# Optimization experiments

Measured on AMD Instinct MI355X. Metric: run time of the kernel, lower is better.

## Reference

```python
import jax, jax.numpy as jnp
import numpy as np

N, E, D_FEAT, D_HID, N_CLASS, N_LAYER = 100000, 1600000, 128, 128, 40, 2


def _sage_layer(x, x_, src, dst, wl, wr, b, n):
    # mean aggregation of neighbor (src) features into dst nodes
    agg = jax.ops.segment_sum(x[src], dst, num_segments=n)          # [N, d_in]
    cnt = jax.ops.segment_sum(jnp.ones((src.shape[0], 1), x.dtype), dst, num_segments=n)
    agg = agg / jnp.maximum(cnt, 1.0)
    h = agg @ wl + x @ wr + b        # neighbor path + root path
    h_ = x_ @ wr + b                 # twin (detached-root) stream: root weight only
    return jax.nn.relu(h), jax.nn.relu(h_)


def setup_inputs() -> dict:
    key = jax.random.key(0)
    ks = jax.random.split(key, 12)
    s = 1.0 / np.sqrt(D_HID)
    inp = {
        "x": jax.random.normal(ks[0], (N, D_FEAT), jnp.float32),
        "edge_index1": jax.random.randint(ks[1], (2, E), 0, N, jnp.int32),
        "edge_index2": jax.random.randint(ks[2], (2, E), 0, N, jnp.int32),
        "wl1": jax.random.uniform(ks[3], (D_FEAT, D_HID), jnp.float32, -s, s),
        "wr1": jax.random.uniform(ks[4], (D_FEAT, D_HID), jnp.float32, -s, s),
        "b1": jnp.zeros((D_HID,), jnp.float32),
        "wl2": jax.random.uniform(ks[5], (D_HID, D_HID), jnp.float32, -s, s),
        "wr2": jax.random.uniform(ks[6], (D_HID, D_HID), jnp.float32, -s, s),
        "b2": jnp.zeros((D_HID,), jnp.float32),
        "w_out": jax.random.uniform(ks[7], (D_HID * N_LAYER, N_CLASS), jnp.float32, -s, s),
        "b_out": jnp.zeros((N_CLASS,), jnp.float32),
        "batch_size": N,
    }
    return inp


def reference(x, edge_index1, edge_index2, wl1, wr1, b1, wl2, wr2, b2, w_out, b_out, batch_size):
    n = x.shape[0]
    x_ = jax.lax.stop_gradient(x)[:batch_size]   # detached twin stream of root nodes
    # layer 1 (dropout is eval-mode no-op)
    h1, h1_ = _sage_layer(x, x_, edge_index1[0], edge_index1[1], wl1, wr1, b1, n)
    # layer 2
    h2, h2_ = _sage_layer(h1, h1_, edge_index2[0], edge_index2[1], wl2, wr2, b2, n)
    # jumping knowledge: mode 'cat' over per-layer root representations
    h = jnp.concatenate([h1[:batch_size], h2[:batch_size]], axis=-1)
    return h @ w_out + b_out
```

## Files before the change

### kernel.cpp

```cpp
#include <hip/hip_runtime.h>


#define MAXB  512
#define CAP   24
#define CAPS  6144
#define PBLK  384

typedef __attribute__((ext_vector_type(8))) short short8;
typedef __attribute__((ext_vector_type(4))) float floatx4;

__device__ __forceinline__ unsigned short f2b(float f) {
    unsigned u = __float_as_uint(f);
    unsigned r = (u + 0x7fffu + ((u >> 16) & 1u)) >> 16;
    return (unsigned short)r;
}
__device__ __forceinline__ float lo2f(unsigned u) { return __uint_as_float(u << 16); }
__device__ __forceinline__ float hi2f(unsigned u) { return __uint_as_float(u & 0xffff0000u); }
__device__ __forceinline__ unsigned pack2(float a, float b) {
    return (unsigned)f2b(a) | ((unsigned)f2b(b) << 16);
}

__global__ __launch_bounds__(256)
void prep_all(const float4* __restrict__ x4, uint4* __restrict__ xb4, long n8,
              const float* __restrict__ wl1, const float* __restrict__ wr1,
              const float* __restrict__ wl2, const float* __restrict__ wr2,
              const float* __restrict__ wo,
              unsigned short* __restrict__ wt1, unsigned short* __restrict__ wt2,
              unsigned short* __restrict__ wot, int* __restrict__ zero_region) {
    long i = (long)blockIdx.x * 256 + threadIdx.x;
    if (i < 2048) zero_region[i] = 0;
    if (i < n8) {
        float4 a = x4[i * 2];
        float4 b = x4[i * 2 + 1];
        uint4 o;
        o.x = pack2(a.x, a.y); o.y = pack2(a.z, a.w);
        o.z = pack2(b.x, b.y); o.w = pack2(b.z, b.w);
        xb4[i] = o;
    }
    if (i < 65536) {
        int l = (int)(i >> 15);
        int k5 = (int)(i & 32767);
        int j = k5 & 7, lane = (k5 >> 3) & 63, kb = (k5 >> 9) & 7, c = k5 >> 12;
        int k = kb * 32 + (lane >> 4) * 8 + j;
        int n = c * 16 + (lane & 15);
        const float* Wl = l ? wl2 : wl1;
        const float* Wr = l ? wr2 : wr1;
        float v = (k < 128) ? Wl[k * 128 + n] : Wr[(k - 128) * 128 + n];
        (l ? wt2 : wt1)[k5] = f2b(v);
    } else if (i < 65536 + 12288) {
        int k5 = (int)(i - 65536);
        int j = k5 & 7, lane = (k5 >> 3) & 63, kb = (k5 >> 9) & 7, c = k5 >> 12;
        int k = kb * 32 + (lane >> 4) * 8 + j;
        int col = c * 16 + (lane & 15);
        float v = (col < 40) ? wo[k * 40 + col] : 0.0f;
        wot[k5] = f2b(v);
    }
}

__global__ __launch_bounds__(256)
void bucket_hist2(const int* __restrict__ dst1, const int* __restrict__ dst2,
                  int* __restrict__ hist1, int* __restrict__ hist2, int E, int nb) {
    __shared__ int h[MAXB];
    const int* dst = blockIdx.y ? dst2 : dst1;
    int* hist      = blockIdx.y ? hist2 : hist1;
    for (int i = threadIdx.x; i < nb; i += 256) h[i] = 0;
    __syncthreads();
    for (int e = blockIdx.x * 256 + threadIdx.x; e < E; e += gridDim.x * 256)
        atomicAdd(&h[dst[e] >> 8], 1);
    __syncthreads();
    for (int i = threadIdx.x; i < nb; i += 256)
        if (h[i]) atomicAdd(&hist[i], h[i]);
}

__global__ __launch_bounds__(256)
void bucket_scan2(const int* __restrict__ hist1, const int* __restrict__ hist2,
                  int* __restrict__ bptr1, int* __restrict__ bptr2, int nb, int E) {
    __shared__ int pair[256];
    const int* hist = blockIdx.x ? hist2 : hist1;
    int* bptr       = blockIdx.x ? bptr2 : bptr1;
    int t = threadIdx.x;
    int v0 = (2 * t < nb) ? hist[2 * t] : 0;
    int v1 = (2 * t + 1 < nb) ? hist[2 * t + 1] : 0;
    pair[t] = v0 + v1;
    __syncthreads();
    for (int off = 1; off < 256; off <<= 1) {
        int y = (t >= off) ? pair[t - off] : 0;
        __syncthreads();
        pair[t] += y;
        __syncthreads();
    }
    int ebase = pair[t] - (v0 + v1);
    if (2 * t < nb)     bptr[2 * t]     = ebase;
    if (2 * t + 1 < nb) bptr[2 * t + 1] = ebase + v0;
    if (t == 0) bptr[nb] = E;
}

__global__ __launch_bounds__(256)
void partition_edges2(const int* __restrict__ ei1, const int* __restrict__ ei2,
                      const int* __restrict__ bptr1, const int* __restrict__ bptr2,
                      int* __restrict__ gcur1, int* __restrict__ gcur2,
                      int* __restrict__ part1, int* __restrict__ part2,
                      int E, int nb) {
    __shared__ unsigned stage[MAXB][CAP];
    __shared__ int lcnt[MAXB];
    const int* src  = blockIdx.y ? ei2 : ei1;
    const int* dst  = src + E;
    const int* bptr = blockIdx.y ? bptr2 : bptr1;
    int* gcur       = blockIdx.y ? gcur2 : gcur1;
    int* part       = blockIdx.y ? part2 : part1;
    const int t = threadIdx.x;
    for (int i = t; i < nb; i += 256) lcnt[i] = 0;
    __syncthreads();
    const int per = (E + gridDim.x - 1) / gridDim.x;
    const int e0 = blockIdx.x * per;
    const int e1 = min(e0 + per, E);
    for (int e = e0 + t; e < e1; e += 256) {
        int d = dst[e];
        int b = d >> 8;
        unsigned rec = (unsigned)src[e] | ((unsigned)(d & 255) << 17);
        int p = atomicAdd(&lcnt[b], 1);
        if (p < CAP) stage[b][p] = rec;
        else {
            int g = atomicAdd(&gcur[b], 1);
            part[bptr[b] + g] = (int)rec;
        }
    }
    __syncthreads();
    for (int b = t; b < nb; b += 256) {
        int c = lcnt[b]; if (c > CAP) c = CAP;
        if (c > 0) {
            int g = atomicAdd(&gcur[b], c);
            int base = bptr[b] + g;
            for (int i = 0; i < c; ++i) part[base + i] = (int)stage[b][i];
        }
    }
}

__global__ __launch_bounds__(256)
void node_sort2(const int* __restrict__ bptr1, const int* __restrict__ bptr2,
                const int* __restrict__ part1, const int* __restrict__ part2,
                int* __restrict__ col1, int* __restrict__ col2,
                int* __restrict__ row_ptr1, int* __restrict__ row_ptr2,
                int N, int E) {
    __shared__ int recs[CAPS];
    __shared__ int sorted[CAPS];
    __shared__ int hcnt[256];
    __shared__ int hoff[256];
    const int* bptr = blockIdx.y ? bptr2 : bptr1;
    const int* part = blockIdx.y ? part2 : part1;
    int* col        = blockIdx.y ? col2 : col1;
    int* row_ptr    = blockIdx.y ? row_ptr2 : row_ptr1;
    const int b = blockIdx.x, t = threadIdx.x;
    const int beg = bptr[b], end = bptr[b + 1];
    int cnt = end - beg;
    if (cnt > CAPS) cnt = CAPS;

    for (int i = t; i < cnt; i += 256) recs[i] = part[beg + i];
    hcnt[t] = 0;
    __syncthreads();
    for (int i = t; i < cnt; i += 256)
        atomicAdd(&hcnt[((unsigned)recs[i]) >> 17], 1);
    __syncthreads();

    int v = hcnt[t];
    hoff[t] = v;
    __syncthreads();
    for (int off = 1; off < 256; off <<= 1) {
        int y = (t >= off) ? hoff[t - off] : 0;
        __syncthreads();
        hoff[t] += y;
        __syncthreads();
    }
    int myoff = hoff[t] - v;

    int row = b * 256 + t;
    if (row <= N) row_ptr[row] = beg + myoff;
    if (b == gridDim.x - 1 && t == 0) row_ptr[N] = E;
    __syncthreads();
    hoff[t] = myoff;
    hcnt[t] = 0;
    __syncthreads();

    for (int i = t; i < cnt; i += 256) {
        unsigned rec = (unsigned)recs[i];
        int node = rec >> 17;
        int p = hoff[node] + atomicAdd(&hcnt[node], 1);
        sorted[p] = (int)(rec & 0x1FFFF);
    }
    __syncthreads();
    for (int i = t; i < cnt; i += 256) col[beg + i] = sorted[i];
}

__global__ __launch_bounds__(256)
void gather_mean_b16(const uint4* __restrict__ xb, const int* __restrict__ row_ptr,
                     const int* __restrict__ col, uint4* __restrict__ agg, int N) {
    int gid  = blockIdx.x * 256 + threadIdx.x;
    int node = gid >> 4;
    int lane = gid & 15;
    if (node >= N) return;
    int beg = row_ptr[node], end = row_ptr[node + 1];
    float acc[8];
#pragma unroll
    for (int j = 0; j < 8; ++j) acc[j] = 0.0f;
    int e = beg;
    for (; e + 7 < end; e += 8) {
        uint4 v[8];
#pragma unroll
        for (int q = 0; q < 8; ++q) v[q] = xb[(size_t)col[e + q] * 16 + lane];
#pragma unroll
        for (int q = 0; q < 8; ++q) {
            acc[0] += lo2f(v[q].x); acc[1] += hi2f(v[q].x);
            acc[2] += lo2f(v[q].y); acc[3] += hi2f(v[q].y);
            acc[4] += lo2f(v[q].z); acc[5] += hi2f(v[q].z);
            acc[6] += lo2f(v[q].w); acc[7] += hi2f(v[q].w);
        }
    }
    for (; e + 3 < end; e += 4) {
        uint4 v[4];
#pragma unroll
        for (int q = 0; q < 4; ++q) v[q] = xb[(size_t)col[e + q] * 16 + lane];
#pragma unroll
        for (int q = 0; q < 4; ++q) {
            acc[0] += lo2f(v[q].x); acc[1] += hi2f(v[q].x);
            acc[2] += lo2f(v[q].y); acc[3] += hi2f(v[q].y);
            acc[4] += lo2f(v[q].z); acc[5] += hi2f(v[q].z);
            acc[6] += lo2f(v[q].w); acc[7] += hi2f(v[q].w);
        }
    }
    for (; e < end; ++e) {
        uint4 v0 = xb[(size_t)col[e] * 16 + lane];
        acc[0] += lo2f(v0.x); acc[1] += hi2f(v0.x);
        acc[2] += lo2f(v0.y); acc[3] += hi2f(v0.y);
        acc[4] += lo2f(v0.z); acc[5] += hi2f(v0.z);
        acc[6] += lo2f(v0.w); acc[7] += hi2f(v0.w);
    }
    float inv = 1.0f / fmaxf((float)(end - beg), 1.0f);
#pragma unroll
    for (int j = 0; j < 8; ++j) acc[j] *= inv;
    uint4 o;
    o.x = pack2(acc[0], acc[1]); o.y = pack2(acc[2], acc[3]);
    o.z = pack2(acc[4], acc[5]); o.w = pack2(acc[6], acc[7]);
    agg[(size_t)node * 16 + lane] = o;
}

__global__ __launch_bounds__(256)
void sage_gemm_mfma(const unsigned short* __restrict__ Aggb,
                    const unsigned short* __restrict__ Xb,
                    const unsigned short* __restrict__ Wt,
                    const float* __restrict__ bias,
                    unsigned short* __restrict__ Hb, int N) {
    const int wave = threadIdx.x >> 6;
    const int lane = threadIdx.x & 63;
    const int quad = lane >> 4;
    const int l16  = lane & 15;
    const int rowbase = blockIdx.x * 128 + wave * 32;

    floatx4 acc[2][8];
#pragma unroll
    for (int r = 0; r < 2; ++r)
#pragma unroll
        for (int c = 0; c < 8; ++c) acc[r][c] = (floatx4){0.f, 0.f, 0.f, 0.f};

    int arow0 = rowbase + l16;      if (arow0 >= N) arow0 = N - 1;
    int arow1 = rowbase + 16 + l16; if (arow1 >= N) arow1 = N - 1;
    const size_t aoff0 = (size_t)arow0 * 128 + quad * 8;
    const size_t aoff1 = (size_t)arow1 * 128 + quad * 8;

#pragma unroll
    for (int kb = 0; kb < 8; ++kb) {
        const unsigned short* Ab = (kb < 4) ? Aggb : Xb;
        const int koff = (kb & 3) * 32;
        short8 a0 = __builtin_bit_cast(short8, *(const uint4*)(Ab + aoff0 + koff));
        short8 a1 = __builtin_bit_cast(short8, *(const uint4*)(Ab + aoff1 + koff));
#pragma unroll
        for (int c = 0; c < 8; ++c) {
            short8 b = __builtin_bit_cast(short8,
                *(const uint4*)(Wt + (size_t)(((c * 8 + kb) * 64 + lane) * 8)));
            acc[0][c] = __builtin_amdgcn_mfma_f32_16x16x32_bf16(a0, b, acc[0][c], 0, 0, 0);
            acc[1][c] = __builtin_amdgcn_mfma_f32_16x16x32_bf16(a1, b, acc[1][c], 0, 0, 0);
        }
    }

    float bcol[8];
#pragma unroll
    for (int c = 0; c < 8; ++c) bcol[c] = bias[c * 16 + l16];
#pragma unroll
    for (int r = 0; r < 2; ++r)
#pragma unroll
        for (int i = 0; i < 4; ++i) {
            int row = rowbase + r * 16 + quad * 4 + i;
            if (row < N) {
#pragma unroll
                for (int c = 0; c < 8; ++c)
                    Hb[(size_t)row * 128 + c * 16 + l16] =
                        f2b(fmaxf(acc[r][c][i] + bcol[c], 0.f));
            }
        }
}

__global__ __launch_bounds__(256)
void out_gemm_mfma(const unsigned short* __restrict__ H1b,
                   const unsigned short* __restrict__ H2b,
                   const unsigned short* __restrict__ Wot,
                   const float* __restrict__ bo,
                   float* __restrict__ out, int N) {
    const int wave = threadIdx.x >> 6;
    const int lane = threadIdx.x & 63;
    const int quad = lane >> 4;
    const int l16  = lane & 15;
    const int rowbase = blockIdx.x * 128 + wave * 32;

    floatx4 acc[2][3];
#pragma unroll
    for (int r = 0; r < 2; ++r)
#pragma unroll
        for (int c = 0; c < 3; ++c) acc[r][c] = (floatx4){0.f, 0.f, 0.f, 0.f};

    int arow0 = rowbase + l16;      if (arow0 >= N) arow0 = N - 1;
    int arow1 = rowbase + 16 + l16; if (arow1 >= N) arow1 = N - 1;
    const size_t aoff0 = (size_t)arow0 * 128 + quad * 8;
    const size_t aoff1 = (size_t)arow1 * 128 + quad * 8;

#pragma unroll
    for (int kb = 0; kb < 8; ++kb) {
        const unsigned short* Ab = (kb < 4) ? H1b : H2b;
        const int koff = (kb & 3) * 32;
        short8 a0 = __builtin_bit_cast(short8, *(const uint4*)(Ab + aoff0 + koff));
        short8 a1 = __builtin_bit_cast(short8, *(const uint4*)(Ab + aoff1 + koff));
#pragma unroll
        for (int c = 0; c < 3; ++c) {
            short8 b = __builtin_bit_cast(short8,
                *(const uint4*)(Wot + (size_t)(((c * 8 + kb) * 64 + lane) * 8)));
            acc[0][c] = __builtin_amdgcn_mfma_f32_16x16x32_bf16(a0, b, acc[0][c], 0, 0, 0);
            acc[1][c] = __builtin_amdgcn_mfma_f32_16x16x32_bf16(a1, b, acc[1][c], 0, 0, 0);
        }
    }

    float bcol[3];
#pragma unroll
    for (int c = 0; c < 3; ++c) {
        int colc = c * 16 + l16;
        bcol[c] = (colc < 40) ? bo[colc] : 0.f;
    }
#pragma unroll
    for (int r = 0; r < 2; ++r)
#pragma unroll
        for (int i = 0; i < 4; ++i) {
            int row = rowbase + r * 16 + quad * 4 + i;
            if (row < N) {
#pragma unroll
                for (int c = 0; c < 3; ++c) {
                    int colc = c * 16 + l16;
                    if (colc < 40)
                        out[(size_t)row * 40 + colc] = acc[r][c][i] + bcol[c];
                }
            }
        }
}

extern "C" void kernel_launch(void* const* d_in, const int* in_sizes, int n_in,
                              void* d_out, int out_size, void* d_ws, size_t ws_size,
                              hipStream_t stream) {
    const float* x     = (const float*)d_in[0];
    const int*   ei1   = (const int*)d_in[1];
    const int*   ei2   = (const int*)d_in[2];
    const float* wl1   = (const float*)d_in[3];
    const float* wr1   = (const float*)d_in[4];
    const float* b1    = (const float*)d_in[5];
    const float* wl2   = (const float*)d_in[6];
    const float* wr2   = (const float*)d_in[7];
    const float* b2    = (const float*)d_in[8];
    const float* w_out = (const float*)d_in[9];
    const float* b_out = (const float*)d_in[10];

    const int N  = in_sizes[0] / 128;
    const int E  = in_sizes[1] / 2;
    const int nb = (N + 255) >> 8;

    int* hist1    = (int*)d_ws;
    int* gcur1    = hist1 + 512;
    int* hist2    = gcur1 + 512;
    int* gcur2    = hist2 + 512;
    int* bptr1    = gcur2 + 512;
    int* bptr2    = bptr1 + 513;
    int* row_ptr1 = bptr2 + 513;
    int* row_ptr2 = row_ptr1 + (N + 1);
    int* part1    = row_ptr2 + (N + 1);
    int* col1     = part1 + E;
    int* part2    = col1 + E;
    int* col2     = part2 + E;
    size_t int_cnt = (size_t)(2048 + 1026 + 2 * (N + 1)) + (size_t)4 * E;
    int_cnt = (int_cnt + 3) & ~(size_t)3;
    unsigned short* xb   = (unsigned short*)((int*)d_ws + int_cnt);
    unsigned short* h1b  = xb  + (size_t)N * 128;
    unsigned short* h2b  = h1b + (size_t)N * 128;
    unsigned short* aggb = h2b + (size_t)N * 128;
    unsigned short* wt1  = aggb + (size_t)N * 128;
    unsigned short* wt2  = wt1 + 32768;
    unsigned short* wot  = wt2 + 32768;

    const long n8         = (long)N * 128 / 8;
    const int prep_blocks = (int)((n8 + 255) / 256);
    const int gath_blocks = (int)(((size_t)N * 16 + 255) / 256);
    const int mfma_blocks = (N + 127) / 128;

    prep_all<<<prep_blocks, 256, 0, stream>>>(
        (const float4*)x, (uint4*)xb, n8, wl1, wr1, wl2, wr2, w_out,
        wt1, wt2, wot, hist1);

    bucket_hist2<<<dim3(256, 2), 256, 0, stream>>>(ei1 + E, ei2 + E, hist1, hist2, E, nb);
    bucket_scan2<<<2, 256, 0, stream>>>(hist1, hist2, bptr1, bptr2, nb, E);
    partition_edges2<<<dim3(PBLK, 2), 256, 0, stream>>>(
        ei1, ei2, bptr1, bptr2, gcur1, gcur2, part1, part2, E, nb);
    node_sort2<<<dim3(nb, 2), 256, 0, stream>>>(
        bptr1, bptr2, part1, part2, col1, col2, row_ptr1, row_ptr2, N, E);

    gather_mean_b16<<<gath_blocks, 256, 0, stream>>>((const uint4*)xb, row_ptr1,
                                                     col1, (uint4*)aggb, N);
    sage_gemm_mfma<<<mfma_blocks, 256, 0, stream>>>(aggb, xb, wt1, b1, h1b, N);
    gather_mean_b16<<<gath_blocks, 256, 0, stream>>>((const uint4*)h1b, row_ptr2,
                                                     col2, (uint4*)aggb, N);
    sage_gemm_mfma<<<mfma_blocks, 256, 0, stream>>>(aggb, h1b, wt2, b2, h2b, N);

    out_gemm_mfma<<<mfma_blocks, 256, 0, stream>>>(h1b, h2b, wot, b_out,
                                                   (float*)d_out, N);
}
```

Baseline: 443.4 us.

## Fuse neighbor gather into SAGE GEMMs and fold output GEMM into layer 2

```diff
diff --git a/kernel.cpp b/kernel.cpp
--- a/kernel.cpp
+++ b/kernel.cpp
@@ -1,10 +1,10 @@
 #include <hip/hip_runtime.h>
 
 
-#define MAXB  512
-#define CAP   24
-#define CAPS  6144
-#define PBLK  384
+#define MAXB 512
+#define CAP  24
+#define CAPS 6144
+#define PBLK 384
 
 typedef __attribute__((ext_vector_type(8))) short short8;
 typedef __attribute__((ext_vector_type(4))) float floatx4;
@@ -191,14 +191,9 @@
     for (int i = t; i < cnt; i += 256) col[beg + i] = sorted[i];
 }
 
-__global__ __launch_bounds__(256)
-void gather_mean_b16(const uint4* __restrict__ xb, const int* __restrict__ row_ptr,
-                     const int* __restrict__ col, uint4* __restrict__ agg, int N) {
-    int gid  = blockIdx.x * 256 + threadIdx.x;
-    int node = gid >> 4;
-    int lane = gid & 15;
-    if (node >= N) return;
-    int beg = row_ptr[node], end = row_ptr[node + 1];
+__device__ __forceinline__ uint4 gather_row(const uint4* __restrict__ xb,
+                                            const int* __restrict__ col,
+                                            int beg, int end, int lane) {
     float acc[8];
 #pragma unroll
     for (int j = 0; j < 8; ++j) acc[j] = 0.0f;
@@ -209,18 +204,6 @@
         for (int q = 0; q < 8; ++q) v[q] = xb[(size_t)col[e + q] * 16 + lane];
 #pragma unroll
         for (int q = 0; q < 8; ++q) {
-            acc[0] += lo2f(v[q].x); acc[1] += hi2f(v[q].x);
-            acc[2] += lo2f(v[q].y); acc[3] += hi2f(v[q].y);
-            acc[4] += lo2f(v[q].z); acc[5] += hi2f(v[q].z);
-            acc[6] += lo2f(v[q].w); acc[7] += hi2f(v[q].w);
-        }
-    }
-    for (; e + 3 < end; e += 4) {
-        uint4 v[4];
-#pragma unroll
-        for (int q = 0; q < 4; ++q) v[q] = xb[(size_t)col[e + q] * 16 + lane];
-#pragma unroll
-        for (int q = 0; q < 4; ++q) {
             acc[0] += lo2f(v[q].x); acc[1] += hi2f(v[q].x);
             acc[2] += lo2f(v[q].y); acc[3] += hi2f(v[q].y);
             acc[4] += lo2f(v[q].z); acc[5] += hi2f(v[q].z);
@@ -240,20 +223,42 @@
     uint4 o;
     o.x = pack2(acc[0], acc[1]); o.y = pack2(acc[2], acc[3]);
     o.z = pack2(acc[4], acc[5]); o.w = pack2(acc[6], acc[7]);
-    agg[(size_t)node * 16 + lane] = o;
-}
-
-__global__ __launch_bounds__(256)
-void sage_gemm_mfma(const unsigned short* __restrict__ Aggb,
-                    const unsigned short* __restrict__ Xb,
-                    const unsigned short* __restrict__ Wt,
-                    const float* __restrict__ bias,
-                    unsigned short* __restrict__ Hb, int N) {
-    const int wave = threadIdx.x >> 6;
-    const int lane = threadIdx.x & 63;
+    return o;
+}
+
+__global__ __launch_bounds__(256)
+void fused_layer1(const uint4* __restrict__ xb4,
+                  const unsigned short* __restrict__ Xb,
+                  const int* __restrict__ row_ptr, const int* __restrict__ col,
+                  const unsigned short* __restrict__ Wt,
+                  const float* __restrict__ bias,
+                  unsigned short* __restrict__ Hb, int N) {
+    __shared__ unsigned short aggL[128][136];
+    const int t = threadIdx.x;
+    const int blockbase = blockIdx.x * 128;
+
+    {
+        const int lane = t & 15;
+        const int nsub = t >> 4;
+#pragma unroll
+        for (int it = 0; it < 8; ++it) {
+            int ln = it * 16 + nsub;
+            int node = blockbase + ln;
+            if (node < N) {
+                int beg = row_ptr[node], end = row_ptr[node + 1];
+                uint4 o = gather_row(xb4, col, beg, end, lane);
+                *(uint4*)&aggL[ln][lane * 8] = o;
+            }
+        }
+    }
+    __syncthreads();
+
+    const int wave = t >> 6;
+    const int lane = t & 63;
     const int quad = lane >> 4;
     const int l16  = lane & 15;
-    const int rowbase = blockIdx.x * 128 + wave * 32;
+    const int lr0 = wave * 32 + l16;
+    const int lr1 = wave * 32 + 16 + l16;
 
     floatx4 acc[2][8];
 #pragma unroll
@@ -261,17 +266,22 @@
 #pragma unroll
         for (int c = 0; c < 8; ++c) acc[r][c] = (floatx4){0.f, 0.f, 0.f, 0.f};
 
-    int arow0 = rowbase + l16;      if (arow0 >= N) arow0 = N - 1;
-    int arow1 = rowbase + 16 + l16; if (arow1 >= N) arow1 = N - 1;
-    const size_t aoff0 = (size_t)arow0 * 128 + quad * 8;
-    const size_t aoff1 = (size_t)arow1 * 128 + quad * 8;
+    int grow0 = blockbase + lr0; if (grow0 >= N) grow0 = N - 1;
+    int grow1 = blockbase + lr1; if (grow1 >= N) grow1 = N - 1;
+    const size_t xoff0 = (size_t)grow0 * 128 + quad * 8;
+    const size_t xoff1 = (size_t)grow1 * 128 + quad * 8;
 
 #pragma unroll
     for (int kb = 0; kb < 8; ++kb) {
-        const unsigned short* Ab = (kb < 4) ? Aggb : Xb;
-        const int koff = (kb & 3) * 32;
-        short8 a0 = __builtin_bit_cast(short8, *(const uint4*)(Ab + aoff0 + koff));
-        short8 a1 = __builtin_bit_cast(short8, *(const uint4*)(Ab + aoff1 + koff));
+        const int koff = (kb & 3) * 32 + quad * 8;
+        short8 a0, a1;
+        if (kb < 4) {
+            a0 = __builtin_bit_cast(short8, *(const uint4*)&aggL[lr0][koff]);
+            a1 = __builtin_bit_cast(short8, *(const uint4*)&aggL[lr1][koff]);
+        } else {
+            a0 = __builtin_bit_cast(short8, *(const uint4*)(Xb + xoff0 + (kb & 3) * 32));
+            a1 = __builtin_bit_cast(short8, *(const uint4*)(Xb + xoff1 + (kb & 3) * 32));
+        }
 #pragma unroll
         for (int c = 0; c < 8; ++c) {
             short8 b = __builtin_bit_cast(short8,
@@ -288,7 +298,7 @@
     for (int r = 0; r < 2; ++r)
 #pragma unroll
         for (int i = 0; i < 4; ++i) {
-            int row = rowbase + r * 16 + quad * 4 + i;
+            int row = blockbase + wave * 32 + r * 16 + quad * 4 + i;
             if (row < N) {
 #pragma unroll
                 for (int c = 0; c < 8; ++c)
@@ -299,40 +309,111 @@
 }
 
 __global__ __launch_bounds__(256)
-void out_gemm_mfma(const unsigned short* __restrict__ H1b,
-                   const unsigned short* __restrict__ H2b,
-                   const unsigned short* __restrict__ Wot,
-                   const float* __restrict__ bo,
-                   float* __restrict__ out, int N) {
-    const int wave = threadIdx.x >> 6;
-    const int lane = threadIdx.x & 63;
+void fused_layer2out(const uint4* __restrict__ h1b4,
+                     const unsigned short* __restrict__ H1b,
+                     const int* __restrict__ row_ptr, const int* __restrict__ col,
+                     const unsigned short* __restrict__ Wt,
+                     const float* __restrict__ bias,
+                     const unsigned short* __restrict__ Wot,
+                     const float* __restrict__ bo,
+                     float* __restrict__ out, int N) {
+    __shared__ unsigned short aggL[128][136];
+    const int t = threadIdx.x;
+    const int blockbase = blockIdx.x * 128;
+
+    {
+        const int lane = t & 15;
+        const int nsub = t >> 4;
+#pragma unroll
+        for (int it = 0; it < 8; ++it) {
+            int ln = it * 16 + nsub;
+            int node = blockbase + ln;
+            if (node < N) {
+                int beg = row_ptr[node], end = row_ptr[node + 1];
+                uint4 o = gather_row(h1b4, col, beg, end, lane);
+                *(uint4*)&aggL[ln][lane * 8] = o;
+            }
+        }
+    }
+    __syncthreads();
+
+    const int wave = t >> 6;
+    const int lane = t & 63;
     const int quad = lane >> 4;
     const int l16  = lane & 15;
-    const int rowbase = blockIdx.x * 128 + wave * 32;
-
-    floatx4 acc[2][3];
+    const int lr0 = wave * 32 + l16;
+    const int lr1 = wave * 32 + 16 + l16;
+
+    int grow0 = blockbase + lr0; if (grow0 >= N) grow0 = N - 1;
+    int grow1 = blockbase + lr1; if (grow1 >= N) grow1 = N - 1;
+    const size_t hoff0 = (size_t)grow0 * 128 + quad * 8;
+    const size_t hoff1 = (size_t)grow1 * 128 + quad * 8;
+
+    floatx4 acc[2][8];
 #pragma unroll
     for (int r = 0; r < 2; ++r)
 #pragma unroll
-        for (int c = 0; c < 3; ++c) acc[r][c] = (floatx4){0.f, 0.f, 0.f, 0.f};
-
-    int arow0 = rowbase + l16;      if (arow0 >= N) arow0 = N - 1;
-    int arow1 = rowbase + 16 + l16; if (arow1 >= N) arow1 = N - 1;
-    const size_t aoff0 = (size_t)arow0 * 128 + quad * 8;
-    const size_t aoff1 = (size_t)arow1 * 128 + quad * 8;
+        for (int c = 0; c < 8; ++c) acc[r][c] = (floatx4){0.f, 0.f, 0.f, 0.f};
 
 #pragma unroll
     for (int kb = 0; kb < 8; ++kb) {
-        const unsigned short* Ab = (kb < 4) ? H1b : H2b;
-        const int koff = (kb & 3) * 32;
-        short8 a0 = __builtin_bit_cast(short8, *(const uint4*)(Ab + aoff0 + koff));
-        short8 a1 = __builtin_bit_cast(short8, *(const uint4*)(Ab + aoff1 + koff));
+        const int koff = (kb & 3) * 32 + quad * 8;
+        short8 a0, a1;
+        if (kb < 4) {
+            a0 = __builtin_bit_cast(short8, *(const uint4*)&aggL[lr0][koff]);
+            a1 = __builtin_bit_cast(short8, *(const uint4*)&aggL[lr1][koff]);
+        } else {
+            a0 = __builtin_bit_cast(short8, *(const uint4*)(H1b + hoff0 + (kb & 3) * 32));
+            a1 = __builtin_bit_cast(short8, *(const uint4*)(H1b + hoff1 + (kb & 3) * 32));
+        }
+#pragma unroll
+        for (int c = 0; c < 8; ++c) {
+            short8 b = __builtin_bit_cast(short8,
+                *(const uint4*)(Wt + (size_t)(((c * 8 + kb) * 64 + lane) * 8)));
+            acc[0][c] = __builtin_amdgcn_mfma_f32_16x16x32_bf16(a0, b, acc[0][c], 0, 0, 0);
+            acc[1][c] = __builtin_amdgcn_mfma_f32_16x16x32_bf16(a1, b, acc[1][c], 0, 0, 0);
+        }
+    }
+
+    {
+        float bcol[8];
+#pragma unroll
+        for (int c = 0; c < 8; ++c) bcol[c] = bias[c * 16 + l16];
+#pragma unroll
+        for (int r = 0; r < 2; ++r)
+#pragma unroll
+            for (int i = 0; i < 4; ++i) {
+                int lrow = wave * 32 + r * 16 + quad * 4 + i;
+#pragma unroll
+                for (int c = 0; c < 8; ++c)
+                    aggL[lrow][c * 16 + l16] =
+                        f2b(fmaxf(acc[r][c][i] + bcol[c], 0.f));
+            }
+    }
+
+    floatx4 acco[2][3];
+#pragma unroll
+    for (int r = 0; r < 2; ++r)
+#pragma unroll
+        for (int c = 0; c < 3; ++c) acco[r][c] = (floatx4){0.f, 0.f, 0.f, 0.f};
+
+#pragma unroll
+    for (int kb = 0; kb < 8; ++kb) {
+        const int koff = (kb & 3) * 32 + quad * 8;
+        short8 a0, a1;
+        if (kb < 4) {
+            a0 = __builtin_bit_cast(short8, *(const uint4*)(H1b + hoff0 + (kb & 3) * 32));
+            a1 = __builtin_bit_cast(short8, *(const uint4*)(H1b + hoff1 + (kb & 3) * 32));
+        } else {
+            a0 = __builtin_bit_cast(short8, *(const uint4*)&aggL[lr0][koff]);
+            a1 = __builtin_bit_cast(short8, *(const uint4*)&aggL[lr1][koff]);
+        }
 #pragma unroll
         for (int c = 0; c < 3; ++c) {
             short8 b = __builtin_bit_cast(short8,
                 *(const uint4*)(Wot + (size_t)(((c * 8 + kb) * 64 + lane) * 8)));
-            acc[0][c] = __builtin_amdgcn_mfma_f32_16x16x32_bf16(a0, b, acc[0][c], 0, 0, 0);
-            acc[1][c] = __builtin_amdgcn_mfma_f32_16x16x32_bf16(a1, b, acc[1][c], 0, 0, 0);
+            acco[0][c] = __builtin_amdgcn_mfma_f32_16x16x32_bf16(a0, b, acco[0][c], 0, 0, 0);
+            acco[1][c] = __builtin_amdgcn_mfma_f32_16x16x32_bf16(a1, b, acco[1][c], 0, 0, 0);
         }
     }
 
@@ -346,13 +427,13 @@
     for (int r = 0; r < 2; ++r)
 #pragma unroll
         for (int i = 0; i < 4; ++i) {
-            int row = rowbase + r * 16 + quad * 4 + i;
+            int row = blockbase + wave * 32 + r * 16 + quad * 4 + i;
             if (row < N) {
 #pragma unroll
                 for (int c = 0; c < 3; ++c) {
                     int colc = c * 16 + l16;
                     if (colc < 40)
-                        out[(size_t)row * 40 + colc] = acc[r][c][i] + bcol[c];
+                        out[(size_t)row * 40 + colc] = acco[r][c][i] + bcol[c];
                 }
             }
         }
@@ -391,17 +472,14 @@
     int* col2     = part2 + E;
     size_t int_cnt = (size_t)(2048 + 1026 + 2 * (N + 1)) + (size_t)4 * E;
     int_cnt = (int_cnt + 3) & ~(size_t)3;
-    unsigned short* xb   = (unsigned short*)((int*)d_ws + int_cnt);
-    unsigned short* h1b  = xb  + (size_t)N * 128;
-    unsigned short* h2b  = h1b + (size_t)N * 128;
-    unsigned short* aggb = h2b + (size_t)N * 128;
-    unsigned short* wt1  = aggb + (size_t)N * 128;
-    unsigned short* wt2  = wt1 + 32768;
-    unsigned short* wot  = wt2 + 32768;
+    unsigned short* xb  = (unsigned short*)((int*)d_ws + int_cnt);
+    unsigned short* h1b = xb  + (size_t)N * 128;
+    unsigned short* wt1 = h1b + (size_t)N * 128;
+    unsigned short* wt2 = wt1 + 32768;
+    unsigned short* wot = wt2 + 32768;
 
     const long n8         = (long)N * 128 / 8;
     const int prep_blocks = (int)((n8 + 255) / 256);
-    const int gath_blocks = (int)(((size_t)N * 16 + 255) / 256);
     const int mfma_blocks = (N + 127) / 128;
 
     prep_all<<<prep_blocks, 256, 0, stream>>>(
@@ -415,13 +493,9 @@
     node_sort2<<<dim3(nb, 2), 256, 0, stream>>>(
         bptr1, bptr2, part1, part2, col1, col2, row_ptr1, row_ptr2, N, E);
 
-    gather_mean_b16<<<gath_blocks, 256, 0, stream>>>((const uint4*)xb, row_ptr1,
-                                                     col1, (uint4*)aggb, N);
-    sage_gemm_mfma<<<mfma_blocks, 256, 0, stream>>>(aggb, xb, wt1, b1, h1b, N);
-    gather_mean_b16<<<gath_blocks, 256, 0, stream>>>((const uint4*)h1b, row_ptr2,
-                                                     col2, (uint4*)aggb, N);
-    sage_gemm_mfma<<<mfma_blocks, 256, 0, stream>>>(aggb, h1b, wt2, b2, h2b, N);
-
-    out_gemm_mfma<<<mfma_blocks, 256, 0, stream>>>(h1b, h2b, wot, b_out,
-                                                   (float*)d_out, N);
-}
+    fused_layer1<<<mfma_blocks, 256, 0, stream>>>(
+        (const uint4*)xb, xb, row_ptr1, col1, wt1, b1, h1b, N);
+    fused_layer2out<<<mfma_blocks, 256, 0, stream>>>(
+        (const uint4*)h1b, h1b, row_ptr2, col2, wt2, b2, wot, b_out,
+        (float*)d_out, N);
+}
```

After: 475.4 us. +7.2%, slower.
